# Optimization experiments

Measured on AMD Instinct MI355X. Metric: run time of the kernel, lower is better.

Reference implementation:

```python
import jax, jax.numpy as jnp
import numpy as np

N = 100000
IN_C = 128
HID = 32
HEADS = 4
E = 1600000
NEG_SLOPE = 0.2


def setup_inputs() -> dict:
    key = jax.random.key(0)
    ks = jax.random.split(key, 12)
    d1 = HEADS * HID  # 128, conv1 output width (concat)
    inp = {
        "x": jax.random.normal(ks[0], (N, IN_C), dtype=jnp.float32),
        "edge_index": jax.random.randint(ks[1], (2, E), 0, N, dtype=jnp.int64),
        # conv1 params: proj [IN_C, HEADS*HID], attention vectors [HEADS, HID]
        "W1": jax.random.normal(ks[2], (IN_C, d1), dtype=jnp.float32) / np.sqrt(IN_C),
        "a1_src": jax.random.normal(ks[3], (HEADS, HID), dtype=jnp.float32) / np.sqrt(HID),
        "a1_dst": jax.random.normal(ks[4], (HEADS, HID), dtype=jnp.float32) / np.sqrt(HID),
        "b1": jnp.zeros((d1,), dtype=jnp.float32),
        # conv2: heads=1, in = out = HEADS*HID
        "W2": jax.random.normal(ks[5], (d1, d1), dtype=jnp.float32) / np.sqrt(d1),
        "a2_src": jax.random.normal(ks[6], (1, d1), dtype=jnp.float32) / np.sqrt(d1),
        "a2_dst": jax.random.normal(ks[7], (1, d1), dtype=jnp.float32) / np.sqrt(d1),
        "b2": jnp.zeros((d1,), dtype=jnp.float32),
    }
    return inp


def gat_conv(x, W, a_src, a_dst, b, src, dst, n_nodes):
    """PyG-style GATConv: proj -> per-edge attention -> segment softmax -> scatter-add."""
    H, C = a_src.shape
    xp = (x @ W).reshape(n_nodes, H, C)           # [N, H, C]
    s_src = jnp.einsum("nhc,hc->nh", xp, a_src)   # [N, H]
    s_dst = jnp.einsum("nhc,hc->nh", xp, a_dst)
    e = jax.nn.leaky_relu(s_src[src] + s_dst[dst], NEG_SLOPE)  # [E, H]
    # numerically stable segment softmax over incoming edges of each dst node
    m = jax.ops.segment_max(e, dst, num_segments=n_nodes)      # [N, H]
    ex = jnp.exp(e - m[dst])
    denom = jax.ops.segment_sum(ex, dst, num_segments=n_nodes) # [N, H]
    alpha = ex / (denom[dst] + 1e-16)                          # [E, H]
    msg = xp[src] * alpha[..., None]                           # [E, H, C]
    out = jax.ops.segment_sum(msg, dst, num_segments=n_nodes)  # [N, H, C]
    return out.reshape(n_nodes, H * C) + b


def reference(x, edge_index, W1, a1_src, a1_dst, b1, W2, a2_src, a2_dst, b2):
    n = x.shape[0]
    # add self loops (PyG GATConv default)
    loop = jnp.arange(n, dtype=edge_index.dtype)
    src = jnp.concatenate([edge_index[0], loop])
    dst = jnp.concatenate([edge_index[1], loop])
    # eval mode: dropout is identity
    h = jax.nn.elu(gat_conv(x, W1, a1_src, a1_dst, b1, src, dst, n))
    out = gat_conv(h, W2, a2_src, a2_dst, b2, src, dst, n)
    return out
```

## Files before the change

kernel.cpp:

```cpp
#include <hip/hip_runtime.h>
#include <hip/hip_fp16.h>

#define D 128
#define LRELU(x) ((x) > 0.f ? (x) : 0.2f * (x))

__global__ void detect_i64(const unsigned int* ei, int* flag) {
    if (threadIdx.x == 0 && blockIdx.x == 0) {
        unsigned int o = 0;
#pragma unroll
        for (int k = 0; k < 64; ++k) o |= ei[2 * k + 1];
        *flag = (o == 0u) ? 1 : 0;
    }
}

__device__ __forceinline__ int load_idx(const void* ei, long long pos, int is64) {
    if (is64) return (int)((const long long*)ei)[pos];
    return ((const int*)ei)[pos];
}

__global__ void hist_kernel(const void* __restrict__ ei, const int* __restrict__ flag,
                            int* __restrict__ count, int* __restrict__ rank, int E) {
    int e = blockIdx.x * blockDim.x + threadIdx.x;
    if (e >= E) return;
    int is64 = *flag;
    int dst = load_idx(ei, (long long)E + e, is64);
    rank[e] = atomicAdd(&count[dst], 1);
}

__global__ void reduce_1024(const int* __restrict__ count, int* __restrict__ bsum, int n) {
    __shared__ int sm[256];
    int t = threadIdx.x, b = blockIdx.x;
    int base = b * 1024 + t * 4;
    int s = 0;
#pragma unroll
    for (int j = 0; j < 4; ++j)
        if (base + j < n) s += count[base + j];
    sm[t] = s;
    __syncthreads();
    for (int of = 128; of >= 1; of >>= 1) {
        if (t < of) sm[t] += sm[t + of];
        __syncthreads();
    }
    if (t == 0) bsum[b] = sm[0];
}

__global__ void scan_partials(int* __restrict__ bsum_ex, const int* __restrict__ bsum, int B) {
    __shared__ int sm[256];
    int t = threadIdx.x;
    int v = (t < B) ? bsum[t] : 0;
    sm[t] = v;
    __syncthreads();
    for (int of = 1; of < 256; of <<= 1) {
        int u = (t >= of) ? sm[t - of] : 0;
        __syncthreads();
        sm[t] += u;
        __syncthreads();
    }
    if (t < B) bsum_ex[t] = sm[t] - v;
}

__global__ void scan_final(const int* __restrict__ count, const int* __restrict__ bsum_ex,
                           int* __restrict__ offsets, int n) {
    __shared__ int sm[256];
    int t = threadIdx.x, b = blockIdx.x;
    int base = b * 1024 + t * 4;
    int c[4];
#pragma unroll
    for (int j = 0; j < 4; ++j) c[j] = (base + j < n) ? count[base + j] : 0;
    int tsum = c[0] + c[1] + c[2] + c[3];
    sm[t] = tsum;
    __syncthreads();
    for (int of = 1; of < 256; of <<= 1) {
        int u = (t >= of) ? sm[t - of] : 0;
        __syncthreads();
        sm[t] += u;
        __syncthreads();
    }
    int o = bsum_ex[b] + sm[t] - tsum;
#pragma unroll
    for (int j = 0; j < 4; ++j) {
        if (base + j < n) offsets[base + j] = o;
        o += c[j];
    }
}

__global__ void scatter_kernel(const void* __restrict__ ei, const int* __restrict__ flag,
                               const int* __restrict__ offsets, const int* __restrict__ rank,
                               int* __restrict__ col, int E) {
    int e = blockIdx.x * blockDim.x + threadIdx.x;
    if (e >= E) return;
    int is64 = *flag;
    int src = load_idx(ei, e, is64);
    int dst = load_idx(ei, (long long)E + e, is64);
    col[offsets[dst] + rank[e]] = src;
}

__launch_bounds__(256, 2)
__global__ void gemm_nn_128(const float* __restrict__ X, const float* __restrict__ W,
                            float* __restrict__ Yp, __half2* __restrict__ Yh, int n) {
    __shared__ float Xt[64][68];
    __shared__ float Wl[64][128];
    const int t = threadIdx.x;
    const int r0 = blockIdx.x * 64;
    const int rb = (t >> 4) * 4;
    const int cb = (t & 15) * 4;
    float acc[4][8] = {};
    for (int ph = 0; ph < 2; ++ph) {
#pragma unroll
        for (int it = 0; it < 4; ++it) {
            int idx = t + it * 256;
            int r = idx >> 4, kq = idx & 15;
            float4 xv = make_float4(0.f, 0.f, 0.f, 0.f);
            if (r0 + r < n)
                xv = *reinterpret_cast<const float4*>(X + (size_t)(r0 + r) * D + ph * 64 + kq * 4);
            Xt[kq * 4 + 0][r] = xv.x;
            Xt[kq * 4 + 1][r] = xv.y;
            Xt[kq * 4 + 2][r] = xv.z;
            Xt[kq * 4 + 3][r] = xv.w;
        }
#pragma unroll
        for (int it = 0; it < 8; ++it) {
            int idx = t + it * 256;
            int k = idx >> 5, c4 = idx & 31;
            *reinterpret_cast<float4*>(&Wl[k][c4 * 4]) =
                *reinterpret_cast<const float4*>(W + (size_t)(ph * 64 + k) * D + c4 * 4);
        }
        __syncthreads();
#pragma unroll 4
        for (int k = 0; k < 64; ++k) {
            float4 a = *reinterpret_cast<const float4*>(&Xt[k][rb]);
            float4 b0 = *reinterpret_cast<const float4*>(&Wl[k][cb]);
            float4 b1 = *reinterpret_cast<const float4*>(&Wl[k][cb + 64]);
            float av[4] = {a.x, a.y, a.z, a.w};
            float bv[8] = {b0.x, b0.y, b0.z, b0.w, b1.x, b1.y, b1.z, b1.w};
#pragma unroll
            for (int i = 0; i < 4; ++i)
#pragma unroll
                for (int j = 0; j < 8; ++j) acc[i][j] = fmaf(av[i], bv[j], acc[i][j]);
        }
        __syncthreads();
    }
#pragma unroll
    for (int i = 0; i < 4; ++i) {
        int row = r0 + rb + i;
        if (row < n) {
            float4 o0 = make_float4(acc[i][0], acc[i][4], acc[i][1], acc[i][5]);
            float4 o1 = make_float4(acc[i][2], acc[i][6], acc[i][3], acc[i][7]);
            *reinterpret_cast<float4*>(Yp + (size_t)row * D + 2 * cb) = o0;
            *reinterpret_cast<float4*>(Yp + (size_t)row * D + 2 * cb + 4) = o1;
            __half2 h[4];
            h[0] = __float22half2_rn(make_float2(acc[i][0], acc[i][4]));
            h[1] = __float22half2_rn(make_float2(acc[i][1], acc[i][5]));
            h[2] = __float22half2_rn(make_float2(acc[i][2], acc[i][6]));
            h[3] = __float22half2_rn(make_float2(acc[i][3], acc[i][7]));
            *reinterpret_cast<float4*>(Yh + (size_t)row * 64 + cb) =
                *reinterpret_cast<const float4*>(h);
        }
    }
}

template <int H>
__launch_bounds__(256)
__global__ void score_kernel(const float* __restrict__ xp2, const float* __restrict__ a_src,
                             const float* __restrict__ a_dst, float* __restrict__ s_src,
                             float* __restrict__ s_dst, int n) {
    int wid = (blockIdx.x * 256 + threadIdx.x) >> 6;
    int lane = threadIdx.x & 63;
    if (wid >= n) return;
    float2 xv = reinterpret_cast<const float2*>(xp2 + (size_t)wid * D)[lane];
    float x0 = xv.x, x1 = xv.y;
    float ps0 = x0 * a_src[lane], ps1 = x1 * a_src[lane + 64];
    float pd0 = x0 * a_dst[lane], pd1 = x1 * a_dst[lane + 64];
    if (H == 4) {
        for (int m = 16; m >= 1; m >>= 1) {
            ps0 += __shfl_xor(ps0, m);
            ps1 += __shfl_xor(ps1, m);
            pd0 += __shfl_xor(pd0, m);
            pd1 += __shfl_xor(pd1, m);
        }
        if (lane == 0) {
            s_src[wid * 4 + 0] = ps0; s_src[wid * 4 + 2] = ps1;
            s_dst[wid * 4 + 0] = pd0; s_dst[wid * 4 + 2] = pd1;
        }
        if (lane == 32) {
            s_src[wid * 4 + 1] = ps0; s_src[wid * 4 + 3] = ps1;
            s_dst[wid * 4 + 1] = pd0; s_dst[wid * 4 + 3] = pd1;
        }
    } else {
        float ps = ps0 + ps1, pd = pd0 + pd1;
        for (int m = 32; m >= 1; m >>= 1) {
            ps += __shfl_xor(ps, m);
            pd += __shfl_xor(pd, m);
        }
        if (lane == 0) { s_src[wid] = ps; s_dst[wid] = pd; }
    }
}

template <int H>
__launch_bounds__(256)
__global__ void stats_weights(const int* __restrict__ col, const int* __restrict__ offsets,
                              const int* __restrict__ deg_arr, const float* __restrict__ s_src,
                              const float* __restrict__ s_dst, float* __restrict__ wbuf,
                              float* __restrict__ swbuf, float* __restrict__ rdbuf, int n) {
    int wid = (blockIdx.x * 256 + threadIdx.x) >> 6;
    int lane = threadIdx.x & 63;
    if (wid >= n) return;
    int off = __builtin_amdgcn_readfirstlane(offsets[wid]);
    int deg = __builtin_amdgcn_readfirstlane(deg_arr[wid]);
    if (H == 4) {
        float4 sdv = *reinterpret_cast<const float4*>(s_dst + (size_t)wid * 4);
        float4 ssv = *reinterpret_cast<const float4*>(s_src + (size_t)wid * 4);
        float es0 = LRELU(ssv.x + sdv.x), es1 = LRELU(ssv.y + sdv.y);
        float es2 = LRELU(ssv.z + sdv.z), es3 = LRELU(ssv.w + sdv.w);
        float m0 = es0, m1 = es1, m2 = es2, m3 = es3;
        for (int i = lane; i < deg; i += 64) {
            int c = col[off + i];
            float4 q = *reinterpret_cast<const float4*>(s_src + (size_t)c * 4);
            float e0 = LRELU(q.x + sdv.x), e1 = LRELU(q.y + sdv.y);
            float e2 = LRELU(q.z + sdv.z), e3 = LRELU(q.w + sdv.w);
            m0 = fmaxf(m0, e0); m1 = fmaxf(m1, e1);
            m2 = fmaxf(m2, e2); m3 = fmaxf(m3, e3);
            *reinterpret_cast<float4*>(wbuf + (size_t)(off + i) * 4) = make_float4(e0, e2, e1, e3);
        }
        for (int s = 32; s >= 1; s >>= 1) {
            m0 = fmaxf(m0, __shfl_xor(m0, s)); m1 = fmaxf(m1, __shfl_xor(m1, s));
            m2 = fmaxf(m2, __shfl_xor(m2, s)); m3 = fmaxf(m3, __shfl_xor(m3, s));
        }
        float s0 = 0.f, s1 = 0.f, s2 = 0.f, s3 = 0.f;
        for (int i = lane; i < deg; i += 64) {
            float4 f = *reinterpret_cast<const float4*>(wbuf + (size_t)(off + i) * 4);
            float w0 = __expf(f.x - m0), w2 = __expf(f.y - m2);
            float w1 = __expf(f.z - m1), w3 = __expf(f.w - m3);
            *reinterpret_cast<float4*>(wbuf + (size_t)(off + i) * 4) = make_float4(w0, w2, w1, w3);
            s0 += w0; s1 += w1; s2 += w2; s3 += w3;
        }
        for (int s = 32; s >= 1; s >>= 1) {
            s0 += __shfl_xor(s0, s); s1 += __shfl_xor(s1, s);
            s2 += __shfl_xor(s2, s); s3 += __shfl_xor(s3, s);
        }
        if (lane == 0) {
            float sw0 = __expf(es0 - m0), sw1 = __expf(es1 - m1);
            float sw2 = __expf(es2 - m2), sw3 = __expf(es3 - m3);
            float r0 = 1.f / (s0 + sw0 + 1e-16f), r1 = 1.f / (s1 + sw1 + 1e-16f);
            float r2 = 1.f / (s2 + sw2 + 1e-16f), r3 = 1.f / (s3 + sw3 + 1e-16f);
            *reinterpret_cast<float4*>(swbuf + (size_t)wid * 4) = make_float4(sw0, sw2, sw1, sw3);
            *reinterpret_cast<float4*>(rdbuf + (size_t)wid * 4) = make_float4(r0, r2, r1, r3);
        }
    } else {
        float sd = s_dst[wid];
        float es = LRELU(s_src[wid] + sd);
        float m = es;
        for (int i = lane; i < deg; i += 64) {
            int c = col[off + i];
            float e = LRELU(s_src[c] + sd);
            m = fmaxf(m, e);
            wbuf[off + i] = e;
        }
        for (int s = 32; s >= 1; s >>= 1) m = fmaxf(m, __shfl_xor(m, s));
        float sum = 0.f;
        for (int i = lane; i < deg; i += 64) {
            float w = __expf(wbuf[off + i] - m);
            wbuf[off + i] = w;
            sum += w;
        }
        for (int s = 32; s >= 1; s >>= 1) sum += __shfl_xor(sum, s);
        if (lane == 0) {
            float sw = __expf(es - m);
            swbuf[wid] = sw;
            rdbuf[wid] = 1.f / (sum + sw + 1e-16f);
        }
    }
}

template <int H, bool DO_ELU>
__launch_bounds__(256)
__global__ void aggregate_w(const int* __restrict__ col, const int* __restrict__ offsets,
                            const int* __restrict__ deg_arr, const float* __restrict__ xp2,
                            const __half2* __restrict__ xph, const float* __restrict__ wbuf,
                            const float* __restrict__ swbuf, const float* __restrict__ rdbuf,
                            const float* __restrict__ bias, float* __restrict__ out, int n) {
    int wid = (blockIdx.x * 256 + threadIdx.x) >> 6;
    int lane = threadIdx.x & 63;
    if (wid >= n) return;
    int off = __builtin_amdgcn_readfirstlane(offsets[wid]);
    int deg = __builtin_amdgcn_readfirstlane(deg_arr[wid]);
    const int half = lane >> 5;
    float swA, swB, rdA, rdB;
    if (H == 4) {
        float2 sw = reinterpret_cast<const float2*>(swbuf)[(size_t)wid * 2 + half];
        float2 rd = reinterpret_cast<const float2*>(rdbuf)[(size_t)wid * 2 + half];
        swA = sw.x; swB = sw.y; rdA = rd.x; rdB = rd.y;
    } else {
        swA = swB = swbuf[wid];
        rdA = rdB = rdbuf[wid];
    }
    float2 xs = reinterpret_cast<const float2*>(xp2 + (size_t)wid * D)[lane];
    float acc0 = swA * xs.x, acc1 = swB * xs.y;

    for (int c0 = 0; c0 < deg; c0 += 64) {
        int rem = deg - c0;
        int cnt = rem < 64 ? rem : 64;
        int vcol = 0;
        float vw = 0.f;
        if (lane < cnt) {
            vcol = col[off + c0 + lane];
            if (H == 1) vw = wbuf[off + c0 + lane];
        }
        auto body = [&](int j) {
            int scol = __builtin_amdgcn_readlane(vcol, j);
            float wA, wB;
            if (H == 4) {
                float2 wv = reinterpret_cast<const float2*>(wbuf)[(size_t)(off + c0 + j) * 2 + half];
                wA = wv.x; wB = wv.y;
            } else {
                wA = wB = __int_as_float(__builtin_amdgcn_readlane(__float_as_int(vw), j));
            }
            float2 xv = __half22float2(xph[(size_t)scol * 64 + lane]);
            acc0 = fmaf(wA, xv.x, acc0);
            acc1 = fmaf(wB, xv.y, acc1);
        };
        int j = 0;
        for (; j + 8 <= cnt; j += 8) {
            body(j); body(j + 1); body(j + 2); body(j + 3);
            body(j + 4); body(j + 5); body(j + 6); body(j + 7);
        }
        for (; j < cnt; ++j) body(j);
    }

    float v0 = acc0 * rdA + bias[lane];
    float v1 = acc1 * rdB + bias[lane + 64];
    if (DO_ELU) {
        v0 = v0 > 0.f ? v0 : expm1f(v0);
        v1 = v1 > 0.f ? v1 : expm1f(v1);
    }
    out[(size_t)wid * D + lane] = v0;
    out[(size_t)wid * D + lane + 64] = v1;
}

extern "C" void kernel_launch(void* const* d_in, const int* in_sizes, int n_in,
                              void* d_out, int out_size, void* d_ws, size_t ws_size,
                              hipStream_t stream) {
    (void)n_in; (void)out_size; (void)ws_size;
    const float* x   = (const float*)d_in[0];
    const void*  ei  = d_in[1];
    const float* W1  = (const float*)d_in[2];
    const float* a1s = (const float*)d_in[3];
    const float* a1d = (const float*)d_in[4];
    const float* b1  = (const float*)d_in[5];
    const float* W2  = (const float*)d_in[6];
    const float* a2s = (const float*)d_in[7];
    const float* a2d = (const float*)d_in[8];
    const float* b2  = (const float*)d_in[9];
    const int N = in_sizes[0] / D;
    const int E = in_sizes[1] / 2;
    float* out = (float*)d_out;

    char* p = (char*)d_ws;
    auto alloc = [&](size_t bytes) {
        char* q = p;
        p += (bytes + 255) & ~(size_t)255;
        return q;
    };
    float*   xp      = (float*)alloc((size_t)N * D * 4);
    __half2* xph     = (__half2*)alloc((size_t)N * 64 * 4);
    float*   ssrc    = (float*)alloc((size_t)N * 4 * 4);
    float*   sdst    = (float*)alloc((size_t)N * 4 * 4);
    float*   swbuf   = (float*)alloc((size_t)N * 4 * 4);
    float*   rdbuf   = (float*)alloc((size_t)N * 4 * 4);
    int*     count   = (int*)alloc((size_t)N * 4);
    int*     offsets = (int*)alloc((size_t)N * 4);
    int*     bsum    = (int*)alloc(256 * 4);
    int*     bsumex  = (int*)alloc(256 * 4);
    int*     flag    = (int*)alloc(256);
    int*     col     = (int*)alloc((size_t)E * 4);
    int*     rank    = (int*)alloc((size_t)E * 4);
    float*   wbuf    = (float*)alloc((size_t)E * 4 * 4);

    hipMemsetAsync(count, 0, (size_t)N * 4, stream);

    detect_i64<<<1, 64, 0, stream>>>((const unsigned int*)ei, flag);
    int eg = (E + 255) / 256;
    hist_kernel<<<eg, 256, 0, stream>>>(ei, flag, count, rank, E);
    int B = (N + 1023) / 1024;
    reduce_1024<<<B, 256, 0, stream>>>(count, bsum, N);
    scan_partials<<<1, 256, 0, stream>>>(bsumex, bsum, B);
    scan_final<<<B, 256, 0, stream>>>(count, bsumex, offsets, N);
    scatter_kernel<<<eg, 256, 0, stream>>>(ei, flag, offsets, rank, col, E);

    int gemmG = (N + 63) / 64;
    int nodeG = (N + 3) / 4;

    gemm_nn_128<<<gemmG, 256, 0, stream>>>(x, W1, xp, xph, N);
    score_kernel<4><<<nodeG, 256, 0, stream>>>(xp, a1s, a1d, ssrc, sdst, N);
    stats_weights<4><<<nodeG, 256, 0, stream>>>(col, offsets, count, ssrc, sdst, wbuf, swbuf, rdbuf, N);
    aggregate_w<4, true><<<nodeG, 256, 0, stream>>>(col, offsets, count, xp, xph, wbuf, swbuf, rdbuf, b1, out, N);

    gemm_nn_128<<<gemmG, 256, 0, stream>>>(out, W2, xp, xph, N);
    score_kernel<1><<<nodeG, 256, 0, stream>>>(xp, a2s, a2d, ssrc, sdst, N);
    stats_weights<1><<<nodeG, 256, 0, stream>>>(col, offsets, count, ssrc, sdst, wbuf, swbuf, rdbuf, N);
    aggregate_w<1, false><<<nodeG, 256, 0, stream>>>(col, offsets, count, xp, xph, wbuf, swbuf, rdbuf, b2, out, N);
}
```

Measured before the change: 607.3 us.

## Fuse softmax stats and aggregation into one per-node kernel, drop edge weight buffer

Merges the stats_weights and aggregate_w kernels into a single per-destination-node wavefront kernel. The per-edge attention scores are recomputed: one pass for the max, and a second inside the aggregation loop where exp weights are computed in registers and broadcast with readlane. This removes the E x 4 float weight buffer with its write/read/rewrite traffic, and one launch per layer. In exchange it gathers s_src twice per edge and adds four readlanes per edge in the inner loop. The unroll factor also drops from 8 to 4.

```diff
diff --git a/kernel.cpp b/kernel.cpp
--- a/kernel.cpp
+++ b/kernel.cpp
@@ -196,17 +196,24 @@
     }
 }
 
-template <int H>
+__device__ __forceinline__ float rl_f(float v, int j) {
+    return __int_as_float(__builtin_amdgcn_readlane(__float_as_int(v), j));
+}
+
+template <int H, bool DO_ELU>
 __launch_bounds__(256)
-__global__ void stats_weights(const int* __restrict__ col, const int* __restrict__ offsets,
-                              const int* __restrict__ deg_arr, const float* __restrict__ s_src,
-                              const float* __restrict__ s_dst, float* __restrict__ wbuf,
-                              float* __restrict__ swbuf, float* __restrict__ rdbuf, int n) {
+__global__ void fused_node(const int* __restrict__ col, const int* __restrict__ offsets,
+                           const int* __restrict__ deg_arr, const float* __restrict__ xp2,
+                           const __half2* __restrict__ xph, const float* __restrict__ s_src,
+                           const float* __restrict__ s_dst, const float* __restrict__ bias,
+                           float* __restrict__ out, int n) {
     int wid = (blockIdx.x * 256 + threadIdx.x) >> 6;
     int lane = threadIdx.x & 63;
     if (wid >= n) return;
     int off = __builtin_amdgcn_readfirstlane(offsets[wid]);
     int deg = __builtin_amdgcn_readfirstlane(deg_arr[wid]);
+    const int hf = lane >> 5;
+
     if (H == 4) {
         float4 sdv = *reinterpret_cast<const float4*>(s_dst + (size_t)wid * 4);
         float4 ssv = *reinterpret_cast<const float4*>(s_src + (size_t)wid * 4);
@@ -216,125 +223,108 @@
         for (int i = lane; i < deg; i += 64) {
             int c = col[off + i];
             float4 q = *reinterpret_cast<const float4*>(s_src + (size_t)c * 4);
-            float e0 = LRELU(q.x + sdv.x), e1 = LRELU(q.y + sdv.y);
-            float e2 = LRELU(q.z + sdv.z), e3 = LRELU(q.w + sdv.w);
-            m0 = fmaxf(m0, e0); m1 = fmaxf(m1, e1);
-            m2 = fmaxf(m2, e2); m3 = fmaxf(m3, e3);
-            *reinterpret_cast<float4*>(wbuf + (size_t)(off + i) * 4) = make_float4(e0, e2, e1, e3);
+            m0 = fmaxf(m0, LRELU(q.x + sdv.x));
+            m1 = fmaxf(m1, LRELU(q.y + sdv.y));
+            m2 = fmaxf(m2, LRELU(q.z + sdv.z));
+            m3 = fmaxf(m3, LRELU(q.w + sdv.w));
         }
         for (int s = 32; s >= 1; s >>= 1) {
             m0 = fmaxf(m0, __shfl_xor(m0, s)); m1 = fmaxf(m1, __shfl_xor(m1, s));
             m2 = fmaxf(m2, __shfl_xor(m2, s)); m3 = fmaxf(m3, __shfl_xor(m3, s));
         }
-        float s0 = 0.f, s1 = 0.f, s2 = 0.f, s3 = 0.f;
-        for (int i = lane; i < deg; i += 64) {
-            float4 f = *reinterpret_cast<const float4*>(wbuf + (size_t)(off + i) * 4);
-            float w0 = __expf(f.x - m0), w2 = __expf(f.y - m2);
-            float w1 = __expf(f.z - m1), w3 = __expf(f.w - m3);
-            *reinterpret_cast<float4*>(wbuf + (size_t)(off + i) * 4) = make_float4(w0, w2, w1, w3);
-            s0 += w0; s1 += w1; s2 += w2; s3 += w3;
+        float sw0 = __expf(es0 - m0), sw1 = __expf(es1 - m1);
+        float sw2 = __expf(es2 - m2), sw3 = __expf(es3 - m3);
+        float2 xs = reinterpret_cast<const float2*>(xp2 + (size_t)wid * D)[lane];
+        float acc0 = (hf ? sw1 : sw0) * xs.x;
+        float acc1 = (hf ? sw3 : sw2) * xs.y;
+        float t0 = 0.f, t1 = 0.f, t2 = 0.f, t3 = 0.f;
+        for (int c0 = 0; c0 < deg; c0 += 64) {
+            int rem = deg - c0;
+            int cnt = rem < 64 ? rem : 64;
+            int vcol = 0;
+            float w0 = 0.f, w1 = 0.f, w2 = 0.f, w3 = 0.f;
+            if (lane < cnt) {
+                vcol = col[off + c0 + lane];
+                float4 q = *reinterpret_cast<const float4*>(s_src + (size_t)vcol * 4);
+                w0 = __expf(LRELU(q.x + sdv.x) - m0);
+                w1 = __expf(LRELU(q.y + sdv.y) - m1);
+                w2 = __expf(LRELU(q.z + sdv.z) - m2);
+                w3 = __expf(LRELU(q.w + sdv.w) - m3);
+                t0 += w0; t1 += w1; t2 += w2; t3 += w3;
+            }
+            auto body = [&](int j) {
+                int scol = __builtin_amdgcn_readlane(vcol, j);
+                float r0 = rl_f(w0, j), r1 = rl_f(w1, j);
+                float r2 = rl_f(w2, j), r3 = rl_f(w3, j);
+                float wA = hf ? r1 : r0;
+                float wB = hf ? r3 : r2;
+                float2 xv = __half22float2(xph[(size_t)scol * 64 + lane]);
+                acc0 = fmaf(wA, xv.x, acc0);
+                acc1 = fmaf(wB, xv.y, acc1);
+            };
+            int j = 0;
+            for (; j + 4 <= cnt; j += 4) { body(j); body(j + 1); body(j + 2); body(j + 3); }
+            for (; j < cnt; ++j) body(j);
         }
         for (int s = 32; s >= 1; s >>= 1) {
-            s0 += __shfl_xor(s0, s); s1 += __shfl_xor(s1, s);
-            s2 += __shfl_xor(s2, s); s3 += __shfl_xor(s3, s);
-        }
-        if (lane == 0) {
-            float sw0 = __expf(es0 - m0), sw1 = __expf(es1 - m1);
-            float sw2 = __expf(es2 - m2), sw3 = __expf(es3 - m3);
-            float r0 = 1.f / (s0 + sw0 + 1e-16f), r1 = 1.f / (s1 + sw1 + 1e-16f);
-            float r2 = 1.f / (s2 + sw2 + 1e-16f), r3 = 1.f / (s3 + sw3 + 1e-16f);
-            *reinterpret_cast<float4*>(swbuf + (size_t)wid * 4) = make_float4(sw0, sw2, sw1, sw3);
-            *reinterpret_cast<float4*>(rdbuf + (size_t)wid * 4) = make_float4(r0, r2, r1, r3);
-        }
+            t0 += __shfl_xor(t0, s); t1 += __shfl_xor(t1, s);
+            t2 += __shfl_xor(t2, s); t3 += __shfl_xor(t3, s);
+        }
+        float rd0 = 1.f / (t0 + sw0 + 1e-16f), rd1 = 1.f / (t1 + sw1 + 1e-16f);
+        float rd2 = 1.f / (t2 + sw2 + 1e-16f), rd3 = 1.f / (t3 + sw3 + 1e-16f);
+        float v0 = acc0 * (hf ? rd1 : rd0) + bias[lane];
+        float v1 = acc1 * (hf ? rd3 : rd2) + bias[lane + 64];
+        if (DO_ELU) {
+            v0 = v0 > 0.f ? v0 : expm1f(v0);
+            v1 = v1 > 0.f ? v1 : expm1f(v1);
+        }
+        out[(size_t)wid * D + lane] = v0;
+        out[(size_t)wid * D + lane + 64] = v1;
     } else {
         float sd = s_dst[wid];
         float es = LRELU(s_src[wid] + sd);
         float m = es;
         for (int i = lane; i < deg; i += 64) {
             int c = col[off + i];
-            float e = LRELU(s_src[c] + sd);
-            m = fmaxf(m, e);
-            wbuf[off + i] = e;
+            m = fmaxf(m, LRELU(s_src[c] + sd));
         }
         for (int s = 32; s >= 1; s >>= 1) m = fmaxf(m, __shfl_xor(m, s));
-        float sum = 0.f;
-        for (int i = lane; i < deg; i += 64) {
-            float w = __expf(wbuf[off + i] - m);
-            wbuf[off + i] = w;
-            sum += w;
-        }
-        for (int s = 32; s >= 1; s >>= 1) sum += __shfl_xor(sum, s);
-        if (lane == 0) {
-            float sw = __expf(es - m);
-            swbuf[wid] = sw;
-            rdbuf[wid] = 1.f / (sum + sw + 1e-16f);
-        }
-    }
-}
-
-template <int H, bool DO_ELU>
-__launch_bounds__(256)
-__global__ void aggregate_w(const int* __restrict__ col, const int* __restrict__ offsets,
-                            const int* __restrict__ deg_arr, const float* __restrict__ xp2,
-                            const __half2* __restrict__ xph, const float* __restrict__ wbuf,
-                            const float* __restrict__ swbuf, const float* __restrict__ rdbuf,
-                            const float* __restrict__ bias, float* __restrict__ out, int n) {
-    int wid = (blockIdx.x * 256 + threadIdx.x) >> 6;
-    int lane = threadIdx.x & 63;
-    if (wid >= n) return;
-    int off = __builtin_amdgcn_readfirstlane(offsets[wid]);
-    int deg = __builtin_amdgcn_readfirstlane(deg_arr[wid]);
-    const int half = lane >> 5;
-    float swA, swB, rdA, rdB;
-    if (H == 4) {
-        float2 sw = reinterpret_cast<const float2*>(swbuf)[(size_t)wid * 2 + half];
-        float2 rd = reinterpret_cast<const float2*>(rdbuf)[(size_t)wid * 2 + half];
-        swA = sw.x; swB = sw.y; rdA = rd.x; rdB = rd.y;
-    } else {
-        swA = swB = swbuf[wid];
-        rdA = rdB = rdbuf[wid];
-    }
-    float2 xs = reinterpret_cast<const float2*>(xp2 + (size_t)wid * D)[lane];
-    float acc0 = swA * xs.x, acc1 = swB * xs.y;
-
-    for (int c0 = 0; c0 < deg; c0 += 64) {
-        int rem = deg - c0;
-        int cnt = rem < 64 ? rem : 64;
-        int vcol = 0;
-        float vw = 0.f;
-        if (lane < cnt) {
-            vcol = col[off + c0 + lane];
-            if (H == 1) vw = wbuf[off + c0 + lane];
-        }
-        auto body = [&](int j) {
-            int scol = __builtin_amdgcn_readlane(vcol, j);
-            float wA, wB;
-            if (H == 4) {
-                float2 wv = reinterpret_cast<const float2*>(wbuf)[(size_t)(off + c0 + j) * 2 + half];
-                wA = wv.x; wB = wv.y;
-            } else {
-                wA = wB = __int_as_float(__builtin_amdgcn_readlane(__float_as_int(vw), j));
+        float sw = __expf(es - m);
+        float2 xs = reinterpret_cast<const float2*>(xp2 + (size_t)wid * D)[lane];
+        float acc0 = sw * xs.x, acc1 = sw * xs.y;
+        float tsum = 0.f;
+        for (int c0 = 0; c0 < deg; c0 += 64) {
+            int rem = deg - c0;
+            int cnt = rem < 64 ? rem : 64;
+            int vcol = 0;
+            float w = 0.f;
+            if (lane < cnt) {
+                vcol = col[off + c0 + lane];
+                w = __expf(LRELU(s_src[vcol] + sd) - m);
+                tsum += w;
             }
-            float2 xv = __half22float2(xph[(size_t)scol * 64 + lane]);
-            acc0 = fmaf(wA, xv.x, acc0);
-            acc1 = fmaf(wB, xv.y, acc1);
-        };
-        int j = 0;
-        for (; j + 8 <= cnt; j += 8) {
-            body(j); body(j + 1); body(j + 2); body(j + 3);
-            body(j + 4); body(j + 5); body(j + 6); body(j + 7);
-        }
-        for (; j < cnt; ++j) body(j);
-    }
-
-    float v0 = acc0 * rdA + bias[lane];
-    float v1 = acc1 * rdB + bias[lane + 64];
-    if (DO_ELU) {
-        v0 = v0 > 0.f ? v0 : expm1f(v0);
-        v1 = v1 > 0.f ? v1 : expm1f(v1);
-    }
-    out[(size_t)wid * D + lane] = v0;
-    out[(size_t)wid * D + lane + 64] = v1;
+            auto body = [&](int j) {
+                int scol = __builtin_amdgcn_readlane(vcol, j);
+                float ww = rl_f(w, j);
+                float2 xv = __half22float2(xph[(size_t)scol * 64 + lane]);
+                acc0 = fmaf(ww, xv.x, acc0);
+                acc1 = fmaf(ww, xv.y, acc1);
+            };
+            int j = 0;
+            for (; j + 4 <= cnt; j += 4) { body(j); body(j + 1); body(j + 2); body(j + 3); }
+            for (; j < cnt; ++j) body(j);
+        }
+        for (int s = 32; s >= 1; s >>= 1) tsum += __shfl_xor(tsum, s);
+        float rd = 1.f / (tsum + sw + 1e-16f);
+        float v0 = acc0 * rd + bias[lane];
+        float v1 = acc1 * rd + bias[lane + 64];
+        if (DO_ELU) {
+            v0 = v0 > 0.f ? v0 : expm1f(v0);
+            v1 = v1 > 0.f ? v1 : expm1f(v1);
+        }
+        out[(size_t)wid * D + lane] = v0;
+        out[(size_t)wid * D + lane + 64] = v1;
+    }
 }
 
 extern "C" void kernel_launch(void* const* d_in, const int* in_sizes, int n_in,
@@ -365,8 +355,6 @@
     __half2* xph     = (__half2*)alloc((size_t)N * 64 * 4);
     float*   ssrc    = (float*)alloc((size_t)N * 4 * 4);
     float*   sdst    = (float*)alloc((size_t)N * 4 * 4);
-    float*   swbuf   = (float*)alloc((size_t)N * 4 * 4);
-    float*   rdbuf   = (float*)alloc((size_t)N * 4 * 4);
     int*     count   = (int*)alloc((size_t)N * 4);
     int*     offsets = (int*)alloc((size_t)N * 4);
     int*     bsum    = (int*)alloc(256 * 4);
@@ -374,7 +362,6 @@
     int*     flag    = (int*)alloc(256);
     int*     col     = (int*)alloc((size_t)E * 4);
     int*     rank    = (int*)alloc((size_t)E * 4);
-    float*   wbuf    = (float*)alloc((size_t)E * 4 * 4);
 
     hipMemsetAsync(count, 0, (size_t)N * 4, stream);
 
@@ -392,11 +379,9 @@
 
     gemm_nn_128<<<gemmG, 256, 0, stream>>>(x, W1, xp, xph, N);
     score_kernel<4><<<nodeG, 256, 0, stream>>>(xp, a1s, a1d, ssrc, sdst, N);
-    stats_weights<4><<<nodeG, 256, 0, stream>>>(col, offsets, count, ssrc, sdst, wbuf, swbuf, rdbuf, N);
-    aggregate_w<4, true><<<nodeG, 256, 0, stream>>>(col, offsets, count, xp, xph, wbuf, swbuf, rdbuf, b1, out, N);
+    fused_node<4, true><<<nodeG, 256, 0, stream>>>(col, offsets, count, xp, xph, ssrc, sdst, b1, out, N);
 
     gemm_nn_128<<<gemmG, 256, 0, stream>>>(out, W2, xp, xph, N);
     score_kernel<1><<<nodeG, 256, 0, stream>>>(xp, a2s, a2d, ssrc, sdst, N);
-    stats_weights<1><<<nodeG, 256, 0, stream>>>(col, offsets, count, ssrc, sdst, wbuf, swbuf, rdbuf, N);
-    aggregate_w<1, false><<<nodeG, 256, 0, stream>>>(col, offsets, count, xp, xph, wbuf, swbuf, rdbuf, b2, out, N);
-}
+    fused_node<1, false><<<nodeG, 256, 0, stream>>>(col, offsets, count, xp, xph, ssrc, sdst, b2, out, N);
+}
```

New measurement: 541.6 us. 10.8% less time.
